# Optimization experiments

Measured on AMD Instinct MI355X. Metric: run time of the kernel, lower is better.

Reference implementation:

```python
import jax, jax.numpy as jnp
import numpy as np

B, S, D = 2, 2048, 768
E, F = 8, 3072  # num_experts, d_ff


def setup_inputs() -> dict:
    key = jax.random.key(0)
    k1, k2, k3, k4 = jax.random.split(key, 4)
    hidden_states = jax.random.normal(k1, (B, S, D), dtype=jnp.float32)
    w_router = jax.random.normal(k2, (D, E), dtype=jnp.float32) * (D ** -0.5)
    w1 = jax.random.normal(k3, (E, D, F), dtype=jnp.float32) * (D ** -0.5)
    w2 = jax.random.normal(k4, (E, F, D), dtype=jnp.float32) * (F ** -0.5)
    return {"hidden_states": hidden_states, "w_router": w_router, "w1": w1, "w2": w2}


def reference(hidden_states, w_router, w1, w2):
    # Router: top-1 (switch) routing.
    router_logits = jnp.einsum("bsd,de->bse", hidden_states, w_router)
    probs = jax.nn.softmax(router_logits, axis=-1)
    expert_index = jnp.argmax(probs, axis=-1)                      # [B,S] int
    router_mask = jax.nn.one_hot(expert_index, E, dtype=hidden_states.dtype)  # [B,S,E]
    router_probs = jnp.max(probs, axis=-1, keepdims=True)          # [B,S,1]

    # Expert FFN dispatch/combine (world_size=1 -> all_to_all is identity):
    # each token is processed by its assigned expert's relu-MLP.
    h1 = jax.nn.relu(jnp.einsum("bsd,edf->ebsf", hidden_states, w1))  # [E,B,S,F]
    h2 = jnp.einsum("ebsf,efd->ebsd", h1, w2)                          # [E,B,S,D]
    expert_out = jnp.einsum("ebsd,bse->bsd", h2, router_mask)          # combine

    out = router_probs * expert_out
    return out, router_logits, expert_index
```

## Files before the change

kernel.cpp:

```cpp
#include <hip/hip_runtime.h>
#include <hip/hip_bf16.h>

#define B_ 2
#define S_ 2048
#define D_ 768
#define E_ 8
#define F_ 3072
#define NT (B_*S_)
#define BM 256
#define BN 128
#define BK 128
#define MAXT 24

typedef __attribute__((ext_vector_type(8))) short bf16x8;
typedef __attribute__((ext_vector_type(4))) float f32x4;
typedef __attribute__((ext_vector_type(8))) unsigned short u16x8;

__device__ __forceinline__ unsigned short f2bf(float f){
  __hip_bfloat16 h = __float2bfloat16(f);
  return *reinterpret_cast<unsigned short*>(&h);
}

__device__ __forceinline__ void gll16(const void* g, void* l){
  __builtin_amdgcn_global_load_lds((const __attribute__((address_space(1))) unsigned int*)g,
                                   (__attribute__((address_space(3))) unsigned int*)l,
                                   16, 0, 0);
}

__global__ __launch_bounds__(256) void router_kernel(
    const float* __restrict__ x, const float* __restrict__ wr,
    float* __restrict__ logits_out, float* __restrict__ idx_out,
    float* __restrict__ probs, int* __restrict__ counts, int* __restrict__ bucket)
{
  __shared__ int sbest[64];
  const int wave = threadIdx.x >> 6, lane = threadIdx.x & 63;
  const int tbase = blockIdx.x * 64 + wave * 16;

  for (int it = 0; it < 16; ++it){
    const int token = tbase + it;
    const float* xp = x + (size_t)token * D_;
    float acc[E_] = {0.f,0.f,0.f,0.f,0.f,0.f,0.f,0.f};
    #pragma unroll
    for (int i = 0; i < 12; ++i){
      const int d = lane + i*64;
      const float v = xp[d];
      const float4 w0 = *(const float4*)(wr + d*8);
      const float4 w1v = *(const float4*)(wr + d*8 + 4);
      acc[0] += v*w0.x; acc[1] += v*w0.y; acc[2] += v*w0.z; acc[3] += v*w0.w;
      acc[4] += v*w1v.x; acc[5] += v*w1v.y; acc[6] += v*w1v.z; acc[7] += v*w1v.w;
    }
    #pragma unroll
    for (int j = 0; j < E_; ++j){
      float a = acc[j];
      for (int off = 32; off > 0; off >>= 1) a += __shfl_xor(a, off);
      acc[j] = a;
    }
    if (lane == 0){
      float m = acc[0];
      #pragma unroll
      for (int j = 1; j < E_; ++j) m = fmaxf(m, acc[j]);
      float p[E_]; float s = 0.f;
      #pragma unroll
      for (int j = 0; j < E_; ++j){ p[j] = expf(acc[j] - m); s += p[j]; }
      const float inv = 1.0f / s;
      int best = 0; float bp = p[0]*inv;
      #pragma unroll
      for (int j = 1; j < E_; ++j){ const float pj = p[j]*inv; if (pj > bp){ bp = pj; best = j; } }
      float* lo = logits_out + (size_t)token * E_;
      #pragma unroll
      for (int j = 0; j < E_; ++j) lo[j] = acc[j];
      idx_out[token] = (float)best;
      probs[token] = bp;
      sbest[wave*16 + it] = best;
    }
  }
  __syncthreads();
  if (threadIdx.x < 64){
    const int l = threadIdx.x;
    const int b = sbest[l];
    unsigned long long m = 0;
    #pragma unroll
    for (int e2 = 0; e2 < E_; ++e2){
      const unsigned long long me = __ballot(b == e2);
      if (b == e2) m = me;
    }
    const int rank = __popcll(m & ((1ull << l) - 1ull));
    const int leader = __ffsll((long long)m) - 1;
    int baseval = 0;
    if (l == leader) baseval = atomicAdd(&counts[b], __popcll(m));
    baseval = __shfl(baseval, leader);
    bucket[b * NT + baseval + rank] = blockIdx.x * 64 + l;
  }
}

__global__ void build_tiles(const int* __restrict__ counts, int* __restrict__ meta)
{
  if (threadIdx.x == 0 && blockIdx.x == 0){
    int off = 0, n = 0;
    for (int e = 0; e < E_; ++e){
      const int c = counts[e];
      meta[1+e] = off;
      const int t = (c + BM - 1) / BM;
      for (int mtt = 0; mtt < t; ++mtt){ meta[16 + n] = (e << 16) | mtt; ++n; }
      off += c;
    }
    meta[0] = n;
  }
}

__global__ __launch_bounds__(256) void gather_cvt(
    const float* __restrict__ x, const int* __restrict__ bucket,
    const int* __restrict__ meta, unsigned short* __restrict__ Ac)
{
  const int wave = threadIdx.x >> 6, lane = threadIdx.x & 63;
  const int i = blockIdx.x * 4 + wave;
  int e = 0;
  #pragma unroll
  for (int k = 1; k < E_; ++k) if (meta[1+k] <= i) e = k;
  const int tok = bucket[e * NT + (i - meta[1+e])];
  const float* src = x + (size_t)tok * D_;
  unsigned short* dst = Ac + (size_t)i * D_;
  #pragma unroll
  for (int p = 0; p < 3; ++p){
    const float4 v = *(const float4*)(src + p*256 + lane*4);
    ushort4 o;
    o.x = f2bf(v.x); o.y = f2bf(v.y); o.z = f2bf(v.z); o.w = f2bf(v.w);
    *(ushort4*)(dst + p*256 + lane*4) = o;
  }
}

__global__ __launch_bounds__(256) void transpose_cvt(
    const float* __restrict__ in, unsigned short* __restrict__ outp, int R, int C)
{
  __shared__ float tile[64][65];
  const int e = blockIdx.z;
  const int r0 = blockIdx.y << 6, c0 = blockIdx.x << 6;
  const float* src = in + (size_t)e * R * C;
  unsigned short* dst = outp + (size_t)e * R * C;
  const int tid = threadIdx.x;
  {
    const int lr = tid >> 4, lc = (tid & 15) << 2;
    #pragma unroll
    for (int rr = 0; rr < 4; ++rr){
      const int row = (rr << 4) + lr;
      const float4 v = *(const float4*)(src + (size_t)(r0 + row) * C + c0 + lc);
      tile[row][lc+0] = v.x; tile[row][lc+1] = v.y;
      tile[row][lc+2] = v.z; tile[row][lc+3] = v.w;
    }
  }
  __syncthreads();
  {
    const int wrr = tid >> 3, wcc = (tid & 7) << 3;
    #pragma unroll
    for (int it = 0; it < 2; ++it){
      const int crow = (it << 5) + wrr;
      u16x8 o;
      #pragma unroll
      for (int j = 0; j < 8; ++j) o[j] = f2bf(tile[wcc + j][crow]);
      *(u16x8*)(dst + (size_t)(c0 + crow) * R + r0 + wcc) = o;
    }
  }
}

template<int KC, int KTOT, int NCOLS, bool RELU, int NSPLIT>
__global__ __launch_bounds__(512) void gemm_g(
    const unsigned short* __restrict__ Ac, const unsigned short* __restrict__ Bt,
    const int* __restrict__ counts, const int* __restrict__ bucket,
    const int* __restrict__ meta, const float* __restrict__ probs,
    unsigned short* __restrict__ h1out, float* __restrict__ fout)
{
  __shared__ unsigned short As[BM*BK];
  __shared__ unsigned short Bs[BN*BK];

  const int nwg = gridDim.x * gridDim.y * gridDim.z;
  const int orig = ((int)blockIdx.z * gridDim.y + blockIdx.y) * gridDim.x + blockIdx.x;
  const int q = nwg >> 3, r = nwg & 7;
  const int xcd = orig & 7, jj = orig >> 3;
  const int wgid = (xcd < r ? xcd*(q+1) : r*(q+1) + (xcd - r)*q) + jj;
  constexpr int NTC = NCOLS / BN;
  const int nt = wgid % NTC;
  const int rest = wgid / NTC;
  const int ks = (NSPLIT > 1) ? (rest % NSPLIT) : 0;
  const int tile = (NSPLIT > 1) ? (rest / NSPLIT) : rest;
  if (tile >= meta[0]) return;

  const int em = meta[16 + tile];
  const int e = em >> 16, mt = em & 0xffff;
  const int cnt = counts[e], off_e = meta[1+e];
  const int rbase = mt * BM;
  const int fbase = nt * BN;
  const int tid = threadIdx.x, wave = tid >> 6, lane = tid & 63;
  const int rsub = lane >> 4;
  const int c16 = lane & 15;
  const int cm1 = cnt - 1;

  const char* Asrc[8]; const char* Bsrc[4];
  #pragma unroll
  for (int c = 0; c < 8; ++c){
    const int row = ((wave + (c << 3)) << 2) + rsub;
    int gr = rbase + row; if (gr > cm1) gr = cm1;
    Asrc[c] = (const char*)(Ac + (size_t)(off_e + gr) * KTOT + ks * KC)
              + ((c16 ^ (row & 15)) << 4);
  }
  #pragma unroll
  for (int c = 0; c < 4; ++c){
    const int row = ((wave + (c << 3)) << 2) + rsub;
    Bsrc[c] = (const char*)(Bt + ((size_t)e * NCOLS + fbase + row) * KTOT + ks * KC)
              + ((c16 ^ (row & 15)) << 4);
  }

  const int wr = (wave >> 1) << 6;
  const int wc = (wave & 1) << 6;
  const int lo16 = lane & 15, hi = lane >> 4;
  f32x4 acc[4][4] = {};
  constexpr int NKT = KC / BK;

  for (int kt = 0; kt < NKT; ++kt){
    const int kb = kt * (BK * 2);
    #pragma unroll
    for (int c = 0; c < 8; ++c)
      gll16(Asrc[c] + kb, (char*)As + ((wave + (c << 3)) << 10));
    #pragma unroll
    for (int c = 0; c < 4; ++c)
      gll16(Bsrc[c] + kb, (char*)Bs + ((wave + (c << 3)) << 10));
    __syncthreads();
    #pragma unroll
    for (int kf = 0; kf < 4; ++kf){
      const int ko = (kf << 6) + (hi << 4);
      bf16x8 af[4], bv[4];
      #pragma unroll
      for (int mf = 0; mf < 4; ++mf){
        const int row = wr + (mf << 4) + lo16;
        af[mf] = *(const bf16x8*)((const char*)As + row * 256 + (ko ^ ((row & 15) << 4)));
      }
      #pragma unroll
      for (int nf = 0; nf < 4; ++nf){
        const int col = wc + (nf << 4) + lo16;
        bv[nf] = *(const bf16x8*)((const char*)Bs + col * 256 + (ko ^ ((col & 15) << 4)));
      }
      #pragma unroll
      for (int mf = 0; mf < 4; ++mf)
        #pragma unroll
        for (int nf = 0; nf < 4; ++nf)
          acc[mf][nf] = __builtin_amdgcn_mfma_f32_16x16x32_bf16(af[mf], bv[nf], acc[mf][nf], 0, 0, 0);
    }
    __syncthreads();
  }

  const int rem = cnt - rbase;
  #pragma unroll
  for (int mf = 0; mf < 4; ++mf){
    #pragma unroll
    for (int j = 0; j < 4; ++j){
      const int rr2 = wr + (mf << 4) + (hi << 2) + j;
      if (rr2 < rem){
        if constexpr (RELU){
          const size_t crow = (size_t)(off_e + rbase + rr2);
          #pragma unroll
          for (int nf = 0; nf < 4; ++nf){
            float v = acc[mf][nf][j];
            v = v > 0.f ? v : 0.f;
            h1out[crow * NCOLS + fbase + wc + (nf << 4) + lo16] = f2bf(v);
          }
        } else {
          const int tok = bucket[e * NT + rbase + rr2];
          const float p = probs[tok];
          #pragma unroll
          for (int nf = 0; nf < 4; ++nf)
            atomicAdd(&fout[(size_t)tok * NCOLS + fbase + wc + (nf << 4) + lo16],
                      p * acc[mf][nf][j]);
        }
      }
    }
  }
}

extern "C" void kernel_launch(void* const* d_in, const int* in_sizes, int n_in,
                              void* d_out, int out_size, void* d_ws, size_t ws_size,
                              hipStream_t stream)
{
  const float* x  = (const float*)d_in[0];
  const float* wr = (const float*)d_in[1];
  const float* w1 = (const float*)d_in[2];
  const float* w2 = (const float*)d_in[3];
  float* out = (float*)d_out;

  constexpr size_t OUT_L = (size_t)NT * D_;
  constexpr size_t OUT_I = OUT_L + (size_t)NT * E_;

  char* ws = (char*)d_ws;
  int*            counts = (int*)ws;
  int*            meta   = (int*)(ws + 256);
  float*          probs  = (float*)(ws + 1024);
  int*            bucket = (int*)(ws + (32u << 10));
  unsigned short* Ac     = (unsigned short*)(ws + (256u << 10));
  unsigned short* w1t    = (unsigned short*)(ws + (8ull  << 20));
  unsigned short* w2t    = (unsigned short*)(ws + (48ull << 20));
  unsigned short* h1c    = (unsigned short*)(ws + (88ull << 20));

  hipMemsetAsync(counts, 0, E_ * sizeof(int), stream);
  hipMemsetAsync(out, 0, OUT_L * sizeof(float), stream);

  router_kernel<<<dim3(NT/64), dim3(256), 0, stream>>>(
      x, wr, out + OUT_L, out + OUT_I, probs, counts, bucket);

  build_tiles<<<dim3(1), dim3(64), 0, stream>>>(counts, meta);

  gather_cvt<<<dim3(NT/4), dim3(256), 0, stream>>>(x, bucket, meta, Ac);

  transpose_cvt<<<dim3(F_/64, D_/64, E_), dim3(256), 0, stream>>>(w1, w1t, D_, F_);
  transpose_cvt<<<dim3(D_/64, F_/64, E_), dim3(256), 0, stream>>>(w2, w2t, F_, D_);

  gemm_g<D_, D_, F_, true, 1><<<dim3(F_/BN, MAXT), dim3(512), 0, stream>>>(
      Ac, w1t, counts, bucket, meta, nullptr, h1c, nullptr);

  gemm_g<F_/2, F_, D_, false, 2><<<dim3(D_/BN, MAXT, 2), dim3(512), 0, stream>>>(
      h1c, w2t, counts, bucket, meta, probs, nullptr, out);
}
```

Before: 362.5 us.

## Double-buffer grouped GEMM LDS with BK=64 and simplify router to per-token atomics

The grouped expert GEMM now uses two LDS buffers with a 64-wide K tile, so the next K tile is loaded while the MFMAs run on the current one, with one barrier per iteration instead of two. The LDS swizzle and load mapping are adjusted for 128-byte rows. The router now handles one token per wave across many more blocks and uses a per-token atomicAdd in place of the ballot-based aggregated append. This trades more atomic contention and a nondeterministic bucket order for more router parallelism.

New measurement: 390.4 us. 1.08x slower.

```diff
diff --git a/kernel.cpp b/kernel.cpp
--- a/kernel.cpp
+++ b/kernel.cpp
@@ -9,7 +9,7 @@
 #define NT (B_*S_)
 #define BM 256
 #define BN 128
-#define BK 128
+#define BK 64
 #define MAXT 24
 
 typedef __attribute__((ext_vector_type(8))) short bf16x8;
@@ -32,64 +32,44 @@
     float* __restrict__ logits_out, float* __restrict__ idx_out,
     float* __restrict__ probs, int* __restrict__ counts, int* __restrict__ bucket)
 {
-  __shared__ int sbest[64];
   const int wave = threadIdx.x >> 6, lane = threadIdx.x & 63;
-  const int tbase = blockIdx.x * 64 + wave * 16;
-
-  for (int it = 0; it < 16; ++it){
-    const int token = tbase + it;
-    const float* xp = x + (size_t)token * D_;
-    float acc[E_] = {0.f,0.f,0.f,0.f,0.f,0.f,0.f,0.f};
-    #pragma unroll
-    for (int i = 0; i < 12; ++i){
-      const int d = lane + i*64;
-      const float v = xp[d];
-      const float4 w0 = *(const float4*)(wr + d*8);
-      const float4 w1v = *(const float4*)(wr + d*8 + 4);
-      acc[0] += v*w0.x; acc[1] += v*w0.y; acc[2] += v*w0.z; acc[3] += v*w0.w;
-      acc[4] += v*w1v.x; acc[5] += v*w1v.y; acc[6] += v*w1v.z; acc[7] += v*w1v.w;
-    }
-    #pragma unroll
-    for (int j = 0; j < E_; ++j){
-      float a = acc[j];
-      for (int off = 32; off > 0; off >>= 1) a += __shfl_xor(a, off);
-      acc[j] = a;
-    }
-    if (lane == 0){
-      float m = acc[0];
-      #pragma unroll
-      for (int j = 1; j < E_; ++j) m = fmaxf(m, acc[j]);
-      float p[E_]; float s = 0.f;
-      #pragma unroll
-      for (int j = 0; j < E_; ++j){ p[j] = expf(acc[j] - m); s += p[j]; }
-      const float inv = 1.0f / s;
-      int best = 0; float bp = p[0]*inv;
-      #pragma unroll
-      for (int j = 1; j < E_; ++j){ const float pj = p[j]*inv; if (pj > bp){ bp = pj; best = j; } }
-      float* lo = logits_out + (size_t)token * E_;
-      #pragma unroll
-      for (int j = 0; j < E_; ++j) lo[j] = acc[j];
-      idx_out[token] = (float)best;
-      probs[token] = bp;
-      sbest[wave*16 + it] = best;
-    }
-  }
-  __syncthreads();
-  if (threadIdx.x < 64){
-    const int l = threadIdx.x;
-    const int b = sbest[l];
-    unsigned long long m = 0;
-    #pragma unroll
-    for (int e2 = 0; e2 < E_; ++e2){
-      const unsigned long long me = __ballot(b == e2);
-      if (b == e2) m = me;
-    }
-    const int rank = __popcll(m & ((1ull << l) - 1ull));
-    const int leader = __ffsll((long long)m) - 1;
-    int baseval = 0;
-    if (l == leader) baseval = atomicAdd(&counts[b], __popcll(m));
-    baseval = __shfl(baseval, leader);
-    bucket[b * NT + baseval + rank] = blockIdx.x * 64 + l;
+  const int token = blockIdx.x * 4 + wave;
+  const float* xp = x + (size_t)token * D_;
+
+  float acc[E_] = {0.f,0.f,0.f,0.f,0.f,0.f,0.f,0.f};
+  #pragma unroll
+  for (int i = 0; i < 12; ++i){
+    const int d = lane + i*64;
+    const float v = xp[d];
+    const float4 w0 = *(const float4*)(wr + d*8);
+    const float4 w1v = *(const float4*)(wr + d*8 + 4);
+    acc[0] += v*w0.x; acc[1] += v*w0.y; acc[2] += v*w0.z; acc[3] += v*w0.w;
+    acc[4] += v*w1v.x; acc[5] += v*w1v.y; acc[6] += v*w1v.z; acc[7] += v*w1v.w;
+  }
+  #pragma unroll
+  for (int j = 0; j < E_; ++j){
+    float a = acc[j];
+    for (int off = 32; off > 0; off >>= 1) a += __shfl_xor(a, off);
+    acc[j] = a;
+  }
+  if (lane == 0){
+    float m = acc[0];
+    #pragma unroll
+    for (int j = 1; j < E_; ++j) m = fmaxf(m, acc[j]);
+    float p[E_]; float s = 0.f;
+    #pragma unroll
+    for (int j = 0; j < E_; ++j){ p[j] = expf(acc[j] - m); s += p[j]; }
+    const float inv = 1.0f / s;
+    int best = 0; float bp = p[0]*inv;
+    #pragma unroll
+    for (int j = 1; j < E_; ++j){ const float pj = p[j]*inv; if (pj > bp){ bp = pj; best = j; } }
+    float* lo = logits_out + (size_t)token * E_;
+    #pragma unroll
+    for (int j = 0; j < E_; ++j) lo[j] = acc[j];
+    idx_out[token] = (float)best;
+    probs[token] = bp;
+    const int pos = atomicAdd(&counts[best], 1);
+    bucket[best * NT + pos] = token;
   }
 }
 
@@ -169,8 +149,8 @@
     const int* __restrict__ meta, const float* __restrict__ probs,
     unsigned short* __restrict__ h1out, float* __restrict__ fout)
 {
-  __shared__ unsigned short As[BM*BK];
-  __shared__ unsigned short Bs[BN*BK];
+  __shared__ unsigned short As[2][BM*BK];
+  __shared__ unsigned short Bs[2][BN*BK];
 
   const int nwg = gridDim.x * gridDim.y * gridDim.z;
   const int orig = ((int)blockIdx.z * gridDim.y + blockIdx.y) * gridDim.x + blockIdx.x;
@@ -190,23 +170,23 @@
   const int rbase = mt * BM;
   const int fbase = nt * BN;
   const int tid = threadIdx.x, wave = tid >> 6, lane = tid & 63;
-  const int rsub = lane >> 4;
-  const int c16 = lane & 15;
+  const int rsub = lane >> 3;
+  const int s8 = lane & 7;
   const int cm1 = cnt - 1;
 
-  const char* Asrc[8]; const char* Bsrc[4];
-  #pragma unroll
-  for (int c = 0; c < 8; ++c){
-    const int row = ((wave + (c << 3)) << 2) + rsub;
+  const char* Asrc[4]; const char* Bsrc[2];
+  #pragma unroll
+  for (int c = 0; c < 4; ++c){
+    const int row = (((c << 3) + wave) << 3) + rsub;
     int gr = rbase + row; if (gr > cm1) gr = cm1;
     Asrc[c] = (const char*)(Ac + (size_t)(off_e + gr) * KTOT + ks * KC)
-              + ((c16 ^ (row & 15)) << 4);
-  }
-  #pragma unroll
-  for (int c = 0; c < 4; ++c){
-    const int row = ((wave + (c << 3)) << 2) + rsub;
+              + ((s8 ^ (row & 7)) << 4);
+  }
+  #pragma unroll
+  for (int c = 0; c < 2; ++c){
+    const int row = (((c << 3) + wave) << 3) + rsub;
     Bsrc[c] = (const char*)(Bt + ((size_t)e * NCOLS + fbase + row) * KTOT + ks * KC)
-              + ((c16 ^ (row & 15)) << 4);
+              + ((s8 ^ (row & 7)) << 4);
   }
 
   const int wr = (wave >> 1) << 6;
@@ -215,28 +195,31 @@
   f32x4 acc[4][4] = {};
   constexpr int NKT = KC / BK;
 
-  for (int kt = 0; kt < NKT; ++kt){
+  auto STAGE = [&](int buf, int kt){
     const int kb = kt * (BK * 2);
     #pragma unroll
-    for (int c = 0; c < 8; ++c)
-      gll16(Asrc[c] + kb, (char*)As + ((wave + (c << 3)) << 10));
+    for (int c = 0; c < 2; ++c)
+      gll16(Bsrc[c] + kb, (char*)&Bs[buf][0] + (((c << 3) + wave) << 10));
     #pragma unroll
     for (int c = 0; c < 4; ++c)
-      gll16(Bsrc[c] + kb, (char*)Bs + ((wave + (c << 3)) << 10));
-    __syncthreads();
-    #pragma unroll
-    for (int kf = 0; kf < 4; ++kf){
+      gll16(Asrc[c] + kb, (char*)&As[buf][0] + (((c << 3) + wave) << 10));
+  };
+  auto COMPUTE = [&](int buf){
+    const char* AsB = (const char*)&As[buf][0];
+    const char* BsB = (const char*)&Bs[buf][0];
+    #pragma unroll
+    for (int kf = 0; kf < 2; ++kf){
       const int ko = (kf << 6) + (hi << 4);
       bf16x8 af[4], bv[4];
       #pragma unroll
       for (int mf = 0; mf < 4; ++mf){
         const int row = wr + (mf << 4) + lo16;
-        af[mf] = *(const bf16x8*)((const char*)As + row * 256 + (ko ^ ((row & 15) << 4)));
+        af[mf] = *(const bf16x8*)(AsB + row * 128 + (ko ^ ((row & 7) << 4)));
       }
       #pragma unroll
       for (int nf = 0; nf < 4; ++nf){
         const int col = wc + (nf << 4) + lo16;
-        bv[nf] = *(const bf16x8*)((const char*)Bs + col * 256 + (ko ^ ((col & 15) << 4)));
+        bv[nf] = *(const bf16x8*)(BsB + col * 128 + (ko ^ ((col & 7) << 4)));
       }
       #pragma unroll
       for (int mf = 0; mf < 4; ++mf)
@@ -244,8 +227,18 @@
         for (int nf = 0; nf < 4; ++nf)
           acc[mf][nf] = __builtin_amdgcn_mfma_f32_16x16x32_bf16(af[mf], bv[nf], acc[mf][nf], 0, 0, 0);
     }
+  };
+
+  STAGE(0, 0);
+  __syncthreads();
+  int cur = 0;
+  for (int kt = 0; kt < NKT - 1; ++kt){
+    STAGE(cur ^ 1, kt + 1);
+    COMPUTE(cur);
     __syncthreads();
-  }
+    cur ^= 1;
+  }
+  COMPUTE(cur);
 
   const int rem = cnt - rbase;
   #pragma unroll
@@ -301,7 +294,7 @@
   hipMemsetAsync(counts, 0, E_ * sizeof(int), stream);
   hipMemsetAsync(out, 0, OUT_L * sizeof(float), stream);
 
-  router_kernel<<<dim3(NT/64), dim3(256), 0, stream>>>(
+  router_kernel<<<dim3(NT/4), dim3(256), 0, stream>>>(
       x, wr, out + OUT_L, out + OUT_I, probs, counts, bucket);
 
   build_tiles<<<dim3(1), dim3(64), 0, stream>>>(counts, meta);
```
